# Optimization experiments

Hardware: AMD Instinct MI355X
Metric: run time of the kernel (lower is better)

The kernel has to match this reference:

```python
import jax, jax.numpy as jnp
import numpy as np

N_USER = 100000
N_ITEM = 100000
E = 500000
EMB, HID, OUT = 128, 128, 64


def _mean_agg(msg_src, src, dst, n_dst):
    """Gather per-edge messages from src nodes, segment-mean onto dst nodes."""
    m = msg_src[src]  # [E, d]
    s = jax.ops.segment_sum(m, dst, num_segments=n_dst)
    cnt = jax.ops.segment_sum(jnp.ones((src.shape[0],), m.dtype), dst,
                              num_segments=n_dst)
    # DGL mean reducer yields 0 for nodes with no in-edges
    return jnp.where(cnt[:, None] > 0, s / jnp.maximum(cnt, 1.0)[:, None], 0.0)


def _layer(feat_u, feat_i, W0, b0, Wui, bui, Wiu, biu,
           src_ui, dst_ui, src_iu, dst_iu):
    # shared self-transform (weight0) -> residual h0 on every ntype
    h0_u = feat_u @ W0 + b0
    h0_i = feat_i @ W0 + b0
    # per-etype transform of source features
    wh_u = feat_u @ Wui + bui  # messages along user->item
    wh_i = feat_i @ Wiu + biu  # messages along item->user
    h_i = _mean_agg(wh_u, src_ui, dst_ui, N_ITEM) + h0_i
    h_u = _mean_agg(wh_i, src_iu, dst_iu, N_USER) + h0_u
    return h_u, h_i


def setup_inputs() -> dict:
    key = jax.random.key(0)
    ks = jax.random.split(key, 12)
    sc_e = 1.0 / np.sqrt(EMB)
    sc_h = 1.0 / np.sqrt(HID)
    return {
        "emb_user": jax.random.normal(ks[0], (N_USER, EMB), jnp.float32),
        "emb_item": jax.random.normal(ks[1], (N_ITEM, EMB), jnp.float32),
        "W1_0": jax.random.normal(ks[2], (EMB, HID), jnp.float32) * sc_e,
        "b1_0": jnp.zeros((HID,), jnp.float32),
        "W1_ui": jax.random.normal(ks[3], (EMB, HID), jnp.float32) * sc_e,
        "b1_ui": jnp.zeros((HID,), jnp.float32),
        "W1_iu": jax.random.normal(ks[4], (EMB, HID), jnp.float32) * sc_e,
        "b1_iu": jnp.zeros((HID,), jnp.float32),
        "W2_0": jax.random.normal(ks[5], (HID, OUT), jnp.float32) * sc_h,
        "b2_0": jnp.zeros((OUT,), jnp.float32),
        "W2_ui": jax.random.normal(ks[6], (HID, OUT), jnp.float32) * sc_h,
        "b2_ui": jnp.zeros((OUT,), jnp.float32),
        "W2_iu": jax.random.normal(ks[7], (HID, OUT), jnp.float32) * sc_h,
        "b2_iu": jnp.zeros((OUT,), jnp.float32),
        "src_ui": jax.random.randint(ks[8], (E,), 0, N_USER, jnp.int32),
        "dst_ui": jax.random.randint(ks[9], (E,), 0, N_ITEM, jnp.int32),
        "src_iu": jax.random.randint(ks[10], (E,), 0, N_ITEM, jnp.int32),
        "dst_iu": jax.random.randint(ks[11], (E,), 0, N_USER, jnp.int32),
    }


def reference(emb_user, emb_item,
              W1_0, b1_0, W1_ui, b1_ui, W1_iu, b1_iu,
              W2_0, b2_0, W2_ui, b2_ui, W2_iu, b2_iu,
              src_ui, dst_ui, src_iu, dst_iu):
    h_u, h_i = _layer(emb_user, emb_item, W1_0, b1_0, W1_ui, b1_ui,
                      W1_iu, b1_iu, src_ui, dst_ui, src_iu, dst_iu)
    h_u = jax.nn.leaky_relu(h_u, 0.01)  # torch F.leaky_relu default slope
    h_i = jax.nn.leaky_relu(h_i, 0.01)
    h_u, h_i = _layer(h_u, h_i, W2_0, b2_0, W2_ui, b2_ui,
                      W2_iu, b2_iu, src_ui, dst_ui, src_iu, dst_iu)
    return h_u, h_i
```

## Files before the change

### kernel.cpp

```cpp
#include <hip/hip_runtime.h>

#define N_USER 100000
#define N_ITEM 100000
#define NEDGE  500000
#define DEGCAP 32

typedef __attribute__((ext_vector_type(8))) short short8;
typedef __attribute__((ext_vector_type(4))) float f32x4;

__device__ __forceinline__ unsigned short f2bf(float f) {
  union { float f; unsigned int u; } x{f};
  unsigned int r = x.u + 0x7fffu + ((x.u >> 16) & 1u);
  return (unsigned short)(r >> 16);
}
__device__ __forceinline__ float bf2f(unsigned short u) {
  union { unsigned int u; float f; } x{(unsigned int)u << 16};
  return x.f;
}

__global__ __launch_bounds__(256) void setup_k(
    const int* __restrict__ src_ui, const int* __restrict__ dst_ui,
    int* __restrict__ cur_i, int* __restrict__ csr_ui,
    const int* __restrict__ src_iu, const int* __restrict__ dst_iu,
    int* __restrict__ cur_u, int* __restrict__ csr_iu,
    const float* __restrict__ emb_u, const float* __restrict__ emb_i,
    unsigned short* __restrict__ ebu, unsigned short* __restrict__ ebi,
    const float* __restrict__ W10, const float* __restrict__ W1ui,
    const float* __restrict__ W1iu, const float* __restrict__ W20,
    const float* __restrict__ W2ui, const float* __restrict__ W2iu,
    unsigned short* __restrict__ WT1i, unsigned short* __restrict__ WT1u,
    unsigned short* __restrict__ WT2i, unsigned short* __restrict__ WT2u) {
  int b = blockIdx.x, tid = threadIdx.x;
  if (b < 3908) {
    const int *src, *dst; int *cur, *csr;
    int bb = b;
    if (bb < 1954) { src = src_ui; dst = dst_ui; cur = cur_i; csr = csr_ui; }
    else { bb -= 1954; src = src_iu; dst = dst_iu; cur = cur_u; csr = csr_iu; }
    int e = bb * 256 + tid;
    if (e < NEDGE) {
      int d = dst[e];
      int p = atomicAdd(&cur[d], 1);
      if (p < DEGCAP) csr[d * DEGCAP + p] = src[e];
    }
  } else if (b < 16408) {
    int blk = b - 3908;
    const float* src; unsigned short* dstp;
    if (blk < 6250) { src = emb_u; dstp = ebu; }
    else { blk -= 6250; src = emb_i; dstp = ebi; }
    size_t base = (size_t)blk * 2048 + (size_t)tid * 8;
    float4 x = *(const float4*)(src + base);
    float4 y = *(const float4*)(src + base + 4);
    short8 v{(short)f2bf(x.x), (short)f2bf(x.y), (short)f2bf(x.z), (short)f2bf(x.w),
             (short)f2bf(y.x), (short)f2bf(y.y), (short)f2bf(y.z), (short)f2bf(y.w)};
    *(short8*)(dstp + base) = v;
  } else {
    int t = (b - 16408) * 256 + tid;
    if (t < 32768) {
      int n = t >> 8, k = t & 255;
      float v = (k < 128) ? W10[k * 128 + n] : W1ui[(k - 128) * 128 + n];
      WT1i[t] = f2bf(v);
    } else if (t < 65536) {
      int q = t - 32768; int n = q >> 8, k = q & 255;
      float v = (k < 128) ? W10[k * 128 + n] : W1iu[(k - 128) * 128 + n];
      WT1u[q] = f2bf(v);
    } else if (t < 81920) {
      int q = t - 65536; int n = q >> 8, k = q & 255;
      float v = (k < 128) ? W20[k * 64 + n] : W2ui[(k - 128) * 64 + n];
      WT2i[q] = f2bf(v);
    } else {
      int q = t - 81920; int n = q >> 8, k = q & 255;
      float v = (k < 128) ? W20[k * 64 + n] : W2iu[(k - 128) * 64 + n];
      WT2u[q] = f2bf(v);
    }
  }
}

__global__ __launch_bounds__(256) void agg2_k(
    const unsigned short* __restrict__ featA, const int* __restrict__ curA,
    const int* __restrict__ csrA, unsigned short* __restrict__ outA,
    const unsigned short* __restrict__ featB, const int* __restrict__ curB,
    const int* __restrict__ csrB, unsigned short* __restrict__ outB,
    int nbA) {
  int b = blockIdx.x;
  const unsigned short* feat; const int* cur; const int* csr; unsigned short* out;
  if (b < nbA) { feat = featA; cur = curA; csr = csrA; out = outA; }
  else { b -= nbA; feat = featB; cur = curB; csr = csrB; out = outB; }
  int node = b * 16 + (threadIdx.x >> 4);
  int ln = threadIdx.x & 15;
  int deg = min(cur[node], DEGCAP);
  const int* cp = csr + (size_t)node * DEGCAP;
  float a[8] = {0, 0, 0, 0, 0, 0, 0, 0};
  int j = 0;
  if (j + 4 <= deg) {
    int i0 = cp[0], i1 = cp[1], i2 = cp[2], i3 = cp[3];
    for (;;) {
      bool more = (j + 8 <= deg);
      int n0, n1, n2, n3;
      if (more) { n0 = cp[j + 4]; n1 = cp[j + 5]; n2 = cp[j + 6]; n3 = cp[j + 7]; }
      short8 v0 = *(const short8*)(feat + (size_t)i0 * 128 + ln * 8);
      short8 v1 = *(const short8*)(feat + (size_t)i1 * 128 + ln * 8);
      short8 v2 = *(const short8*)(feat + (size_t)i2 * 128 + ln * 8);
      short8 v3 = *(const short8*)(feat + (size_t)i3 * 128 + ln * 8);
#pragma unroll
      for (int d = 0; d < 8; ++d)
        a[d] += (bf2f((unsigned short)v0[d]) + bf2f((unsigned short)v1[d])) +
                (bf2f((unsigned short)v2[d]) + bf2f((unsigned short)v3[d]));
      j += 4;
      if (!more) break;
      i0 = n0; i1 = n1; i2 = n2; i3 = n3;
    }
  }
  if (j + 2 <= deg) {
    int i0 = cp[j], i1 = cp[j + 1];
    short8 v0 = *(const short8*)(feat + (size_t)i0 * 128 + ln * 8);
    short8 v1 = *(const short8*)(feat + (size_t)i1 * 128 + ln * 8);
#pragma unroll
    for (int d = 0; d < 8; ++d)
      a[d] += bf2f((unsigned short)v0[d]) + bf2f((unsigned short)v1[d]);
    j += 2;
  }
  if (j < deg) {
    short8 v = *(const short8*)(feat + (size_t)cp[j] * 128 + ln * 8);
#pragma unroll
    for (int d = 0; d < 8; ++d) a[d] += bf2f((unsigned short)v[d]);
  }
  float sc = deg ? 1.f / (float)deg : 0.f;
  short8 pk;
#pragma unroll
  for (int d = 0; d < 8; ++d) pk[d] = (short)f2bf(a[d] * sc);
  *(short8*)(out + (size_t)node * 128 + ln * 8) = pk;
}

template <int N, bool LRELU, bool OUTBF16>
__global__ __launch_bounds__(256) void gemm2_k(
    const unsigned short* __restrict__ A1a, const unsigned short* __restrict__ A2a,
    const unsigned short* __restrict__ WTa, const float* __restrict__ b0a,
    const float* __restrict__ bea, const int* __restrict__ cura,
    void* __restrict__ outa,
    const unsigned short* __restrict__ A1b, const unsigned short* __restrict__ A2b,
    const unsigned short* __restrict__ WTb, const float* __restrict__ b0b,
    const float* __restrict__ beb, const int* __restrict__ curb,
    void* __restrict__ outb, int M, int nbA) {
  constexpr int BM = 64;
  constexpr int CPW = N / 4;
  constexpr int NCF = CPW / 16;
  __shared__ short As[BM * 128];
  __shared__ short Ws[N * 128];
  __shared__ float degmask[BM];

  int blk = blockIdx.x;
  const unsigned short* A1; const unsigned short* A2; const unsigned short* WT;
  const float* b0; const float* be; const int* cur; void* outv;
  if (blk < nbA) { A1 = A1a; A2 = A2a; WT = WTa; b0 = b0a; be = bea; cur = cura; outv = outa; }
  else { blk -= nbA; A1 = A1b; A2 = A2b; WT = WTb; b0 = b0b; be = beb; cur = curb; outv = outb; }

  const int tid = threadIdx.x;
  const int lane = tid & 63;
  const int wave = tid >> 6;
  const int row0 = blk * BM;
  const int colbase = wave * CPW;

  if (tid < BM) {
    int r = row0 + tid;
    degmask[tid] = (r < M && cur[r] > 0) ? 1.f : 0.f;
  }

  f32x4 acc[4][NCF] = {};

#pragma unroll
  for (int kh = 0; kh < 2; ++kh) {
    __syncthreads();
    const unsigned short* base = (kh == 0) ? A1 : A2;
#pragma unroll
    for (int it = 0; it < 4; ++it) {
      int chunk = tid + it * 256;
      int row = chunk >> 4, c16 = chunk & 15;
      int gr = row0 + row; if (gr > M - 1) gr = M - 1;
      short8 v = *(const short8*)(base + (size_t)gr * 128 + c16 * 8);
      int byteoff = row * 256 + ((c16 * 16) ^ ((row & 7) << 4));
      *(short8*)((char*)As + byteoff) = v;
    }
#pragma unroll
    for (int it = 0; it < (N * 16) / 256; ++it) {
      int chunk = tid + it * 256;
      int n = chunk >> 4, c16 = chunk & 15;
      short8 v = *(const short8*)(WT + (size_t)n * 256 + kh * 128 + c16 * 8);
      int byteoff = n * 256 + ((c16 * 16) ^ ((n & 7) << 4));
      *(short8*)((char*)Ws + byteoff) = v;
    }
    __syncthreads();

#pragma unroll
    for (int ks = 0; ks < 4; ++ks) {
      short8 af[4];
#pragma unroll
      for (int rf = 0; rf < 4; ++rf) {
        int row = rf * 16 + (lane & 15);
        int c16 = ks * 4 + (lane >> 4);
        int byteoff = row * 256 + ((c16 * 16) ^ ((row & 7) << 4));
        af[rf] = *(const short8*)((const char*)As + byteoff);
      }
      short8 wf[NCF];
#pragma unroll
      for (int cf = 0; cf < NCF; ++cf) {
        int n = colbase + cf * 16 + (lane & 15);
        int c16 = ks * 4 + (lane >> 4);
        int byteoff = n * 256 + ((c16 * 16) ^ ((n & 7) << 4));
        wf[cf] = *(const short8*)((const char*)Ws + byteoff);
      }
#pragma unroll
      for (int rf = 0; rf < 4; ++rf)
#pragma unroll
        for (int cf = 0; cf < NCF; ++cf)
          acc[rf][cf] = __builtin_amdgcn_mfma_f32_16x16x32_bf16(
              af[rf], wf[cf], acc[rf][cf], 0, 0, 0);
    }
  }

#pragma unroll
  for (int cf = 0; cf < NCF; ++cf) {
    int c = colbase + cf * 16 + (lane & 15);
    float bb0 = b0[c], bbe = be[c];
#pragma unroll
    for (int rf = 0; rf < 4; ++rf) {
#pragma unroll
      for (int j = 0; j < 4; ++j) {
        int lr = rf * 16 + (lane >> 4) * 4 + j;
        int r = row0 + lr;
        if (r < M) {
          float v = acc[rf][cf][j] + bb0 + degmask[lr] * bbe;
          if (LRELU) v = (v >= 0.f) ? v : 0.01f * v;
          if (OUTBF16)
            ((unsigned short*)outv)[(size_t)r * N + c] = f2bf(v);
          else
            ((float*)outv)[(size_t)r * N + c] = v;
        }
      }
    }
  }
}

extern "C" void kernel_launch(void* const* d_in, const int* in_sizes, int n_in,
                              void* d_out, int out_size, void* d_ws,
                              size_t ws_size, hipStream_t stream) {
  const float* emb_u = (const float*)d_in[0];
  const float* emb_i = (const float*)d_in[1];
  const float* W1_0  = (const float*)d_in[2];
  const float* b1_0  = (const float*)d_in[3];
  const float* W1_ui = (const float*)d_in[4];
  const float* b1_ui = (const float*)d_in[5];
  const float* W1_iu = (const float*)d_in[6];
  const float* b1_iu = (const float*)d_in[7];
  const float* W2_0  = (const float*)d_in[8];
  const float* b2_0  = (const float*)d_in[9];
  const float* W2_ui = (const float*)d_in[10];
  const float* b2_ui = (const float*)d_in[11];
  const float* W2_iu = (const float*)d_in[12];
  const float* b2_iu = (const float*)d_in[13];
  const int* src_ui = (const int*)d_in[14];
  const int* dst_ui = (const int*)d_in[15];
  const int* src_iu = (const int*)d_in[16];
  const int* dst_iu = (const int*)d_in[17];
  float* out = (float*)d_out;

  char* p = (char*)d_ws;
  unsigned short* WT1i = (unsigned short*)p; p += 65536;
  unsigned short* WT1u = (unsigned short*)p; p += 65536;
  unsigned short* WT2i = (unsigned short*)p; p += 32768;
  unsigned short* WT2u = (unsigned short*)p; p += 32768;
  int* cur_i = (int*)p; p += 400128;
  int* cur_u = (int*)p; p += 400128;
  int* csr_ui = (int*)p; p += (size_t)100032 * DEGCAP * 4;
  int* csr_iu = (int*)p; p += (size_t)100032 * DEGCAP * 4;
  const size_t FB = (size_t)N_USER * 128 * 2;
  unsigned short* ebu  = (unsigned short*)p; p += FB;
  unsigned short* ebi  = (unsigned short*)p; p += FB;
  unsigned short* aggA = (unsigned short*)p; p += FB;
  unsigned short* aggB = (unsigned short*)p; p += FB;
  unsigned short* hu = ebu;
  unsigned short* hi = ebi;

  const int GG = (N_USER + 63) / 64;

  hipMemsetAsync(cur_i, 0, 2 * 400128, stream);
  setup_k<<<16792, 256, 0, stream>>>(src_ui, dst_ui, cur_i, csr_ui,
                                     src_iu, dst_iu, cur_u, csr_iu,
                                     emb_u, emb_i, ebu, ebi,
                                     W1_0, W1_ui, W1_iu, W2_0, W2_ui, W2_iu,
                                     WT1i, WT1u, WT2i, WT2u);

  agg2_k<<<2 * 6250, 256, 0, stream>>>(
      ebu, cur_i, csr_ui, aggA, ebi, cur_u, csr_iu, aggB, 6250);
  gemm2_k<128, true, true><<<2 * GG, 256, 0, stream>>>(
      ebi, aggA, WT1i, b1_0, b1_ui, cur_i, hi,
      ebu, aggB, WT1u, b1_0, b1_iu, cur_u, hu, N_USER, GG);

  agg2_k<<<2 * 6250, 256, 0, stream>>>(
      hu, cur_i, csr_ui, aggA, hi, cur_u, csr_iu, aggB, 6250);
  gemm2_k<64, false, false><<<2 * GG, 256, 0, stream>>>(
      hi, aggA, WT2i, b2_0, b2_ui, cur_i, out + (size_t)N_USER * 64,
      hu, aggB, WT2u, b2_0, b2_iu, cur_u, out, N_USER, GG);
}
```

Before: 253.7 us.

## Move layer-1 self-transform GEMM into setup kernel, interleaved with CSR fill

The layer-1 self term (emb @ W0 + b0) is now computed in the setup kernel, with block indices interleaved across edge-fill, self-GEMM, conversion and weight-transpose roles so the compute-bound GEMM can overlap the atomic-heavy CSR build. The layer-1 GEMM after aggregation then only multiplies the aggregated half (K=128) and adds the precomputed h0, halving its work on the critical path. h0 is staged in the output buffer before that buffer is overwritten by layer 2, and the CSR writes use nontemporal stores. The cost is extra h0 traffic (write plus read back) and a larger, more divergent setup kernel.

```diff
diff --git a/kernel.cpp b/kernel.cpp
--- a/kernel.cpp
+++ b/kernel.cpp
@@ -5,6 +5,12 @@
 #define NEDGE  500000
 #define DEGCAP 32
 
+#define B_FILL 3908
+#define B_GEMM 3126
+#define B_CONV 12500
+#define B_WT   384
+#define B_TOT  (B_FILL + B_GEMM + B_CONV + B_WT)
+
 typedef __attribute__((ext_vector_type(8))) short short8;
 typedef __attribute__((ext_vector_type(4))) float f32x4;
 
@@ -18,7 +24,7 @@
   return x.f;
 }
 
-__global__ __launch_bounds__(256) void setup_k(
+__global__ __launch_bounds__(256, 4) void phase1_k(
     const int* __restrict__ src_ui, const int* __restrict__ dst_ui,
     int* __restrict__ cur_i, int* __restrict__ csr_ui,
     const int* __restrict__ src_iu, const int* __restrict__ dst_iu,
@@ -29,48 +35,121 @@
     const float* __restrict__ W1iu, const float* __restrict__ W20,
     const float* __restrict__ W2ui, const float* __restrict__ W2iu,
     unsigned short* __restrict__ WT1i, unsigned short* __restrict__ WT1u,
-    unsigned short* __restrict__ WT2i, unsigned short* __restrict__ WT2u) {
+    unsigned short* __restrict__ WT2i, unsigned short* __restrict__ WT2u,
+    const float* __restrict__ b10,
+    unsigned short* __restrict__ h0u, unsigned short* __restrict__ h0i) {
+  __shared__ short As[64 * 128];
   int b = blockIdx.x, tid = threadIdx.x;
-  if (b < 3908) {
+  int q = b / 5, m = b % 5;
+
+  if (m == 0 && q < B_FILL) {
     const int *src, *dst; int *cur, *csr;
-    int bb = b;
+    int bb = q;
     if (bb < 1954) { src = src_ui; dst = dst_ui; cur = cur_i; csr = csr_ui; }
     else { bb -= 1954; src = src_iu; dst = dst_iu; cur = cur_u; csr = csr_iu; }
     int e = bb * 256 + tid;
     if (e < NEDGE) {
       int d = dst[e];
       int p = atomicAdd(&cur[d], 1);
-      if (p < DEGCAP) csr[d * DEGCAP + p] = src[e];
-    }
-  } else if (b < 16408) {
-    int blk = b - 3908;
-    const float* src; unsigned short* dstp;
-    if (blk < 6250) { src = emb_u; dstp = ebu; }
-    else { blk -= 6250; src = emb_i; dstp = ebi; }
-    size_t base = (size_t)blk * 2048 + (size_t)tid * 8;
-    float4 x = *(const float4*)(src + base);
-    float4 y = *(const float4*)(src + base + 4);
-    short8 v{(short)f2bf(x.x), (short)f2bf(x.y), (short)f2bf(x.z), (short)f2bf(x.w),
-             (short)f2bf(y.x), (short)f2bf(y.y), (short)f2bf(y.z), (short)f2bf(y.w)};
-    *(short8*)(dstp + base) = v;
+      if (p < DEGCAP) __builtin_nontemporal_store(src[e], &csr[d * DEGCAP + p]);
+    }
+  } else if (m == 1 && q < B_GEMM) {
+    const float* A; unsigned short* h0; int blk;
+    if (q < 1563) { A = emb_i; h0 = h0i; blk = q; }
+    else { A = emb_u; h0 = h0u; blk = q - 1563; }
+    int row0 = blk * 64;
+    int lane = tid & 63, wave = tid >> 6;
+    short8 wf[2][4];
+#pragma unroll
+    for (int cf = 0; cf < 2; ++cf) {
+      int n = wave * 32 + cf * 16 + (lane & 15);
+#pragma unroll
+      for (int ks = 0; ks < 4; ++ks) {
+        int k0 = ks * 32 + (lane >> 4) * 8;
+#pragma unroll
+        for (int j = 0; j < 8; ++j)
+          wf[cf][ks][j] = (short)f2bf(W10[(k0 + j) * 128 + n]);
+      }
+    }
+#pragma unroll
+    for (int it = 0; it < 4; ++it) {
+      int chunk = tid + it * 256;
+      int row = chunk >> 4, c16 = chunk & 15;
+      int gr = row0 + row; if (gr > N_USER - 1) gr = N_USER - 1;
+      const float* s = A + (size_t)gr * 128 + c16 * 8;
+      float4 x = *(const float4*)s;
+      float4 y = *(const float4*)(s + 4);
+      short8 v{(short)f2bf(x.x), (short)f2bf(x.y), (short)f2bf(x.z), (short)f2bf(x.w),
+               (short)f2bf(y.x), (short)f2bf(y.y), (short)f2bf(y.z), (short)f2bf(y.w)};
+      int byteoff = row * 256 + ((c16 * 16) ^ ((row & 7) << 4));
+      *(short8*)((char*)As + byteoff) = v;
+    }
+    __syncthreads();
+    f32x4 acc[4][2] = {};
+#pragma unroll
+    for (int ks = 0; ks < 4; ++ks) {
+      short8 af[4];
+#pragma unroll
+      for (int rf = 0; rf < 4; ++rf) {
+        int row = rf * 16 + (lane & 15);
+        int c16 = ks * 4 + (lane >> 4);
+        int byteoff = row * 256 + ((c16 * 16) ^ ((row & 7) << 4));
+        af[rf] = *(const short8*)((const char*)As + byteoff);
+      }
+#pragma unroll
+      for (int rf = 0; rf < 4; ++rf)
+#pragma unroll
+        for (int cf = 0; cf < 2; ++cf)
+          acc[rf][cf] = __builtin_amdgcn_mfma_f32_16x16x32_bf16(
+              af[rf], wf[cf][ks], acc[rf][cf], 0, 0, 0);
+    }
+#pragma unroll
+    for (int cf = 0; cf < 2; ++cf) {
+      int c = wave * 32 + cf * 16 + (lane & 15);
+      float bb0 = b10[c];
+#pragma unroll
+      for (int rf = 0; rf < 4; ++rf)
+#pragma unroll
+        for (int j = 0; j < 4; ++j) {
+          int r = row0 + rf * 16 + (lane >> 4) * 4 + j;
+          if (r < N_USER)
+            h0[(size_t)r * 128 + c] = f2bf(acc[rf][cf][j] + bb0);
+        }
+    }
   } else {
-    int t = (b - 16408) * 256 + tid;
-    if (t < 32768) {
-      int n = t >> 8, k = t & 255;
-      float v = (k < 128) ? W10[k * 128 + n] : W1ui[(k - 128) * 128 + n];
-      WT1i[t] = f2bf(v);
-    } else if (t < 65536) {
-      int q = t - 32768; int n = q >> 8, k = q & 255;
-      float v = (k < 128) ? W10[k * 128 + n] : W1iu[(k - 128) * 128 + n];
-      WT1u[q] = f2bf(v);
-    } else if (t < 81920) {
-      int q = t - 65536; int n = q >> 8, k = q & 255;
-      float v = (k < 128) ? W20[k * 64 + n] : W2ui[(k - 128) * 64 + n];
-      WT2i[q] = f2bf(v);
+    int fills_before = min((b + 4) / 5, B_FILL);
+    int gems_before  = min((b + 3) / 5, B_GEMM);
+    int sr = b - fills_before - gems_before;
+    if (sr < B_CONV) {
+      int blk = sr;
+      const float* src; unsigned short* dstp;
+      if (blk < 6250) { src = emb_u; dstp = ebu; }
+      else { blk -= 6250; src = emb_i; dstp = ebi; }
+      size_t base = (size_t)blk * 2048 + (size_t)tid * 8;
+      float4 x = *(const float4*)(src + base);
+      float4 y = *(const float4*)(src + base + 4);
+      short8 v{(short)f2bf(x.x), (short)f2bf(x.y), (short)f2bf(x.z), (short)f2bf(x.w),
+               (short)f2bf(y.x), (short)f2bf(y.y), (short)f2bf(y.z), (short)f2bf(y.w)};
+      *(short8*)(dstp + base) = v;
     } else {
-      int q = t - 81920; int n = q >> 8, k = q & 255;
-      float v = (k < 128) ? W20[k * 64 + n] : W2iu[(k - 128) * 64 + n];
-      WT2u[q] = f2bf(v);
+      int t = (sr - B_CONV) * 256 + tid;
+      if (t < 32768) {
+        int n = t >> 8, k = t & 255;
+        float v = (k < 128) ? W10[k * 128 + n] : W1ui[(k - 128) * 128 + n];
+        WT1i[t] = f2bf(v);
+      } else if (t < 65536) {
+        int u = t - 32768; int n = u >> 8, k = u & 255;
+        float v = (k < 128) ? W10[k * 128 + n] : W1iu[(k - 128) * 128 + n];
+        WT1u[u] = f2bf(v);
+      } else if (t < 81920) {
+        int u = t - 65536; int n = u >> 8, k = u & 255;
+        float v = (k < 128) ? W20[k * 64 + n] : W2ui[(k - 128) * 64 + n];
+        WT2i[u] = f2bf(v);
+      } else {
+        int u = t - 81920; int n = u >> 8, k = u & 255;
+        float v = (k < 128) ? W20[k * 64 + n] : W2iu[(k - 128) * 64 + n];
+        WT2u[u] = f2bf(v);
+      }
     }
   }
 }
@@ -131,6 +210,100 @@
   *(short8*)(out + (size_t)node * 128 + ln * 8) = pk;
 }
 
+__global__ __launch_bounds__(256) void egemm_k(
+    const unsigned short* __restrict__ A2a, const unsigned short* __restrict__ h0a,
+    const unsigned short* __restrict__ WTa, const float* __restrict__ bea,
+    const int* __restrict__ cura, unsigned short* __restrict__ outa,
+    const unsigned short* __restrict__ A2b, const unsigned short* __restrict__ h0b,
+    const unsigned short* __restrict__ WTb, const float* __restrict__ beb,
+    const int* __restrict__ curb, unsigned short* __restrict__ outb,
+    int nbA) {
+  __shared__ short As[64 * 128];
+  __shared__ short Ws[128 * 128];
+  __shared__ float degmask[64];
+
+  int blk = blockIdx.x;
+  const unsigned short *A2, *h0, *WT; const float* be; const int* cur;
+  unsigned short* outp;
+  if (blk < nbA) { A2 = A2a; h0 = h0a; WT = WTa; be = bea; cur = cura; outp = outa; }
+  else { blk -= nbA; A2 = A2b; h0 = h0b; WT = WTb; be = beb; cur = curb; outp = outb; }
+
+  const int tid = threadIdx.x;
+  const int lane = tid & 63;
+  const int wave = tid >> 6;
+  const int row0 = blk * 64;
+  const int colbase = wave * 32;
+
+  if (tid < 64) {
+    int r = row0 + tid;
+    degmask[tid] = (r < N_USER && cur[r] > 0) ? 1.f : 0.f;
+  }
+#pragma unroll
+  for (int it = 0; it < 4; ++it) {
+    int chunk = tid + it * 256;
+    int row = chunk >> 4, c16 = chunk & 15;
+    int gr = row0 + row; if (gr > N_USER - 1) gr = N_USER - 1;
+    short8 v = *(const short8*)(A2 + (size_t)gr * 128 + c16 * 8);
+    int byteoff = row * 256 + ((c16 * 16) ^ ((row & 7) << 4));
+    *(short8*)((char*)As + byteoff) = v;
+  }
+#pragma unroll
+  for (int it = 0; it < 8; ++it) {
+    int chunk = tid + it * 256;
+    int n = chunk >> 4, c16 = chunk & 15;
+    short8 v = *(const short8*)(WT + (size_t)n * 256 + 128 + c16 * 8);
+    int byteoff = n * 256 + ((c16 * 16) ^ ((n & 7) << 4));
+    *(short8*)((char*)Ws + byteoff) = v;
+  }
+  __syncthreads();
+
+  f32x4 acc[4][2] = {};
+#pragma unroll
+  for (int ks = 0; ks < 4; ++ks) {
+    short8 af[4];
+#pragma unroll
+    for (int rf = 0; rf < 4; ++rf) {
+      int row = rf * 16 + (lane & 15);
+      int c16 = ks * 4 + (lane >> 4);
+      int byteoff = row * 256 + ((c16 * 16) ^ ((row & 7) << 4));
+      af[rf] = *(const short8*)((const char*)As + byteoff);
+    }
+    short8 wfr[2];
+#pragma unroll
+    for (int cf = 0; cf < 2; ++cf) {
+      int n = colbase + cf * 16 + (lane & 15);
+      int c16 = ks * 4 + (lane >> 4);
+      int byteoff = n * 256 + ((c16 * 16) ^ ((n & 7) << 4));
+      wfr[cf] = *(const short8*)((const char*)Ws + byteoff);
+    }
+#pragma unroll
+    for (int rf = 0; rf < 4; ++rf)
+#pragma unroll
+      for (int cf = 0; cf < 2; ++cf)
+        acc[rf][cf] = __builtin_amdgcn_mfma_f32_16x16x32_bf16(
+            af[rf], wfr[cf], acc[rf][cf], 0, 0, 0);
+  }
+
+#pragma unroll
+  for (int cf = 0; cf < 2; ++cf) {
+    int c = colbase + cf * 16 + (lane & 15);
+    float bbe = be[c];
+#pragma unroll
+    for (int rf = 0; rf < 4; ++rf)
+#pragma unroll
+      for (int j = 0; j < 4; ++j) {
+        int lr = rf * 16 + (lane >> 4) * 4 + j;
+        int r = row0 + lr;
+        if (r < N_USER) {
+          float v = acc[rf][cf][j] + bf2f(h0[(size_t)r * 128 + c]) +
+                    degmask[lr] * bbe;
+          v = (v >= 0.f) ? v : 0.01f * v;
+          outp[(size_t)r * 128 + c] = f2bf(v);
+        }
+      }
+  }
+}
+
 template <int N, bool LRELU, bool OUTBF16>
 __global__ __launch_bounds__(256) void gemm2_k(
     const unsigned short* __restrict__ A1a, const unsigned short* __restrict__ A2a,
@@ -277,27 +450,26 @@
   unsigned short* ebi  = (unsigned short*)p; p += FB;
   unsigned short* aggA = (unsigned short*)p; p += FB;
   unsigned short* aggB = (unsigned short*)p; p += FB;
-  unsigned short* hu = ebu;
-  unsigned short* hi = ebi;
-
-  const int GG = (N_USER + 63) / 64;
+  unsigned short* h0u = (unsigned short*)d_out;
+  unsigned short* h0i = h0u + (size_t)N_USER * 128;
 
   hipMemsetAsync(cur_i, 0, 2 * 400128, stream);
-  setup_k<<<16792, 256, 0, stream>>>(src_ui, dst_ui, cur_i, csr_ui,
-                                     src_iu, dst_iu, cur_u, csr_iu,
-                                     emb_u, emb_i, ebu, ebi,
-                                     W1_0, W1_ui, W1_iu, W2_0, W2_ui, W2_iu,
-                                     WT1i, WT1u, WT2i, WT2u);
+  phase1_k<<<B_TOT, 256, 0, stream>>>(
+      src_ui, dst_ui, cur_i, csr_ui, src_iu, dst_iu, cur_u, csr_iu,
+      emb_u, emb_i, ebu, ebi,
+      W1_0, W1_ui, W1_iu, W2_0, W2_ui, W2_iu,
+      WT1i, WT1u, WT2i, WT2u, b1_0, h0u, h0i);
 
   agg2_k<<<2 * 6250, 256, 0, stream>>>(
       ebu, cur_i, csr_ui, aggA, ebi, cur_u, csr_iu, aggB, 6250);
-  gemm2_k<128, true, true><<<2 * GG, 256, 0, stream>>>(
-      ebi, aggA, WT1i, b1_0, b1_ui, cur_i, hi,
-      ebu, aggB, WT1u, b1_0, b1_iu, cur_u, hu, N_USER, GG);
+  egemm_k<<<2 * 1563, 256, 0, stream>>>(
+      aggA, h0i, WT1i, b1_ui, cur_i, ebi,
+      aggB, h0u, WT1u, b1_iu, cur_u, ebu,
+      1563);
 
   agg2_k<<<2 * 6250, 256, 0, stream>>>(
-      hu, cur_i, csr_ui, aggA, hi, cur_u, csr_iu, aggB, 6250);
-  gemm2_k<64, false, false><<<2 * GG, 256, 0, stream>>>(
-      hi, aggA, WT2i, b2_0, b2_ui, cur_i, out + (size_t)N_USER * 64,
-      hu, aggB, WT2u, b2_0, b2_iu, cur_u, out, N_USER, GG);
-}
+      ebu, cur_i, csr_ui, aggA, ebi, cur_u, csr_iu, aggB, 6250);
+  gemm2_k<64, false, false><<<2 * 1563, 256, 0, stream>>>(
+      ebi, aggA, WT2i, b2_0, b2_ui, cur_i, out + (size_t)N_USER * 64,
+      ebu, aggB, WT2u, b2_0, b2_iu, cur_u, out, N_USER, 1563);
+}
```

Result: slower. 279.8 us (+10.3%).

## Shard CSR build counters into four replicas and compact neighbor lists in LDS

Applied to the files above, without the earlier changes.

The CSR build now spreads each destination's atomic counter across four replicas, each with its own 16-slot bucket. Each thread handles four edges and writes neighbors with nontemporal stores, and setup blocks are scrambled so fill, convert and weight-transpose work interleave. The aggregation kernel loads the 64-slot row, prefix-scans the replica counts within each 16-lane group, and compacts the indices into LDS before gathering. The aggregation scratch buffers now alias the output buffer, which cuts workspace traffic but depends on each GEMM block reading its aggregated rows before overwriting the same bytes.

```diff
diff --git a/kernel.cpp b/kernel.cpp
--- a/kernel.cpp
+++ b/kernel.cpp
@@ -3,7 +3,13 @@
 #define N_USER 100000
 #define N_ITEM 100000
 #define NEDGE  500000
-#define DEGCAP 32
+#define CURS   100032
+#define RCAP   16
+
+#define B_FILL 978
+#define B_CONV 12500
+#define B_WT   384
+#define B_TOT  (B_FILL + B_CONV + B_WT)
 
 typedef __attribute__((ext_vector_type(8))) short short8;
 typedef __attribute__((ext_vector_type(4))) float f32x4;
@@ -30,31 +36,48 @@
     const float* __restrict__ W2ui, const float* __restrict__ W2iu,
     unsigned short* __restrict__ WT1i, unsigned short* __restrict__ WT1u,
     unsigned short* __restrict__ WT2i, unsigned short* __restrict__ WT2u) {
-  int b = blockIdx.x, tid = threadIdx.x;
-  if (b < 3908) {
+  int b = (int)(((unsigned long long)blockIdx.x * 7919ull) % (unsigned long long)B_TOT);
+  int tid = threadIdx.x;
+  if (b < B_FILL) {
     const int *src, *dst; int *cur, *csr;
     int bb = b;
-    if (bb < 1954) { src = src_ui; dst = dst_ui; cur = cur_i; csr = csr_ui; }
-    else { bb -= 1954; src = src_iu; dst = dst_iu; cur = cur_u; csr = csr_iu; }
-    int e = bb * 256 + tid;
-    if (e < NEDGE) {
-      int d = dst[e];
-      int p = atomicAdd(&cur[d], 1);
-      if (p < DEGCAP) csr[d * DEGCAP + p] = src[e];
-    }
-  } else if (b < 16408) {
-    int blk = b - 3908;
+    if (bb < 489) { src = src_ui; dst = dst_ui; cur = cur_i; csr = csr_ui; }
+    else { bb -= 489; src = src_iu; dst = dst_iu; cur = cur_u; csr = csr_iu; }
+    int e0 = bb * 1024 + tid;
+    int d[4], s[4];
+    bool ok[4];
+#pragma unroll
+    for (int k = 0; k < 4; ++k) {
+      int e = e0 + k * 256;
+      ok[k] = (e < NEDGE);
+      d[k] = ok[k] ? dst[e] : 0;
+      s[k] = ok[k] ? src[e] : 0;
+    }
+    int p[4];
+#pragma unroll
+    for (int k = 0; k < 4; ++k) {
+      int rk = (tid + k) & 3;
+      p[k] = ok[k] ? atomicAdd(&cur[rk * CURS + d[k]], 1) : RCAP;
+    }
+#pragma unroll
+    for (int k = 0; k < 4; ++k) {
+      int rk = (tid + k) & 3;
+      if (ok[k] && p[k] < RCAP)
+        __builtin_nontemporal_store(s[k], &csr[d[k] * 64 + rk * RCAP + p[k]]);
+    }
+  } else if (b < B_FILL + B_CONV) {
+    int blk = b - B_FILL;
     const float* src; unsigned short* dstp;
     if (blk < 6250) { src = emb_u; dstp = ebu; }
     else { blk -= 6250; src = emb_i; dstp = ebi; }
-    size_t base = (size_t)blk * 2048 + (size_t)tid * 8;
-    float4 x = *(const float4*)(src + base);
-    float4 y = *(const float4*)(src + base + 4);
+    size_t g = (size_t)blk * 2048 + (size_t)tid * 8;
+    float4 x = *(const float4*)(src + g);
+    float4 y = *(const float4*)(src + g + 4);
     short8 v{(short)f2bf(x.x), (short)f2bf(x.y), (short)f2bf(x.z), (short)f2bf(x.w),
              (short)f2bf(y.x), (short)f2bf(y.y), (short)f2bf(y.z), (short)f2bf(y.w)};
-    *(short8*)(dstp + base) = v;
+    *(short8*)(dstp + g) = v;
   } else {
-    int t = (b - 16408) * 256 + tid;
+    int t = (b - B_FILL - B_CONV) * 256 + tid;
     if (t < 32768) {
       int n = t >> 8, k = t & 255;
       float v = (k < 128) ? W10[k * 128 + n] : W1ui[(k - 128) * 128 + n];
@@ -75,28 +98,49 @@
   }
 }
 
-__global__ __launch_bounds__(256) void agg2_k(
+__global__ __launch_bounds__(256) void aggc_k(
     const unsigned short* __restrict__ featA, const int* __restrict__ curA,
     const int* __restrict__ csrA, unsigned short* __restrict__ outA,
     const unsigned short* __restrict__ featB, const int* __restrict__ curB,
     const int* __restrict__ csrB, unsigned short* __restrict__ outB,
     int nbA) {
+  __shared__ int sidx[16][64];
   int b = blockIdx.x;
   const unsigned short* feat; const int* cur; const int* csr; unsigned short* out;
   if (b < nbA) { feat = featA; cur = curA; csr = csrA; out = outA; }
   else { b -= nbA; feat = featB; cur = curB; csr = csrB; out = outB; }
-  int node = b * 16 + (threadIdx.x >> 4);
-  int ln = threadIdx.x & 15;
-  int deg = min(cur[node], DEGCAP);
-  const int* cp = csr + (size_t)node * DEGCAP;
+  int grp = threadIdx.x >> 4;
+  int ln  = threadIdx.x & 15;
+  int node = b * 16 + grp;
+
+  int4 sl = *(const int4*)(csr + (size_t)node * 64 + ln * 4);
+  int cr = cur[(size_t)(ln >> 2) * CURS + node];
+  cr = min(cr, RCAP);
+  int m = cr - (ln & 3) * 4;
+  m = m < 0 ? 0 : (m > 4 ? 4 : m);
+  int pre = m;
+#pragma unroll
+  for (int d = 1; d < 16; d <<= 1) {
+    int t = __shfl_up(pre, d, 16);
+    if (ln >= d) pre += t;
+  }
+  int start = pre - m;
+  int deg = __shfl(pre, 15, 16);
+  if (m > 0) sidx[grp][start] = sl.x;
+  if (m > 1) sidx[grp][start + 1] = sl.y;
+  if (m > 2) sidx[grp][start + 2] = sl.z;
+  if (m > 3) sidx[grp][start + 3] = sl.w;
+  __syncthreads();
+
+  const int* lidx = sidx[grp];
   float a[8] = {0, 0, 0, 0, 0, 0, 0, 0};
   int j = 0;
   if (j + 4 <= deg) {
-    int i0 = cp[0], i1 = cp[1], i2 = cp[2], i3 = cp[3];
+    int i0 = lidx[0], i1 = lidx[1], i2 = lidx[2], i3 = lidx[3];
     for (;;) {
       bool more = (j + 8 <= deg);
       int n0, n1, n2, n3;
-      if (more) { n0 = cp[j + 4]; n1 = cp[j + 5]; n2 = cp[j + 6]; n3 = cp[j + 7]; }
+      if (more) { n0 = lidx[j + 4]; n1 = lidx[j + 5]; n2 = lidx[j + 6]; n3 = lidx[j + 7]; }
       short8 v0 = *(const short8*)(feat + (size_t)i0 * 128 + ln * 8);
       short8 v1 = *(const short8*)(feat + (size_t)i1 * 128 + ln * 8);
       short8 v2 = *(const short8*)(feat + (size_t)i2 * 128 + ln * 8);
@@ -111,7 +155,7 @@
     }
   }
   if (j + 2 <= deg) {
-    int i0 = cp[j], i1 = cp[j + 1];
+    int i0 = lidx[j], i1 = lidx[j + 1];
     short8 v0 = *(const short8*)(feat + (size_t)i0 * 128 + ln * 8);
     short8 v1 = *(const short8*)(feat + (size_t)i1 * 128 + ln * 8);
 #pragma unroll
@@ -120,7 +164,7 @@
     j += 2;
   }
   if (j < deg) {
-    short8 v = *(const short8*)(feat + (size_t)cp[j] * 128 + ln * 8);
+    short8 v = *(const short8*)(feat + (size_t)lidx[j] * 128 + ln * 8);
 #pragma unroll
     for (int d = 0; d < 8; ++d) a[d] += bf2f((unsigned short)v[d]);
   }
@@ -162,7 +206,10 @@
 
   if (tid < BM) {
     int r = row0 + tid;
-    degmask[tid] = (r < M && cur[r] > 0) ? 1.f : 0.f;
+    int ds = 0;
+    if (r < M)
+      ds = cur[r] + cur[CURS + r] + cur[2 * CURS + r] + cur[3 * CURS + r];
+    degmask[tid] = (ds > 0) ? 1.f : 0.f;
   }
 
   f32x4 acc[4][NCF] = {};
@@ -268,34 +315,34 @@
   unsigned short* WT1u = (unsigned short*)p; p += 65536;
   unsigned short* WT2i = (unsigned short*)p; p += 32768;
   unsigned short* WT2u = (unsigned short*)p; p += 32768;
-  int* cur_i = (int*)p; p += 400128;
-  int* cur_u = (int*)p; p += 400128;
-  int* csr_ui = (int*)p; p += (size_t)100032 * DEGCAP * 4;
-  int* csr_iu = (int*)p; p += (size_t)100032 * DEGCAP * 4;
+  int* cur_i = (int*)p; p += 4 * CURS * 4;
+  int* cur_u = (int*)p; p += 4 * CURS * 4;
+  int* csr_ui = (int*)p; p += (size_t)CURS * 64 * 4;
+  int* csr_iu = (int*)p; p += (size_t)CURS * 64 * 4;
   const size_t FB = (size_t)N_USER * 128 * 2;
   unsigned short* ebu  = (unsigned short*)p; p += FB;
   unsigned short* ebi  = (unsigned short*)p; p += FB;
-  unsigned short* aggA = (unsigned short*)p; p += FB;
-  unsigned short* aggB = (unsigned short*)p; p += FB;
   unsigned short* hu = ebu;
   unsigned short* hi = ebi;
+  unsigned short* aggB = (unsigned short*)out;
+  unsigned short* aggA = (unsigned short*)(out + (size_t)N_USER * 64);
 
   const int GG = (N_USER + 63) / 64;
 
-  hipMemsetAsync(cur_i, 0, 2 * 400128, stream);
-  setup_k<<<16792, 256, 0, stream>>>(src_ui, dst_ui, cur_i, csr_ui,
+  hipMemsetAsync(cur_i, 0, 2 * 4 * CURS * 4, stream);
+  setup_k<<<B_TOT, 256, 0, stream>>>(src_ui, dst_ui, cur_i, csr_ui,
                                      src_iu, dst_iu, cur_u, csr_iu,
                                      emb_u, emb_i, ebu, ebi,
                                      W1_0, W1_ui, W1_iu, W2_0, W2_ui, W2_iu,
                                      WT1i, WT1u, WT2i, WT2u);
 
-  agg2_k<<<2 * 6250, 256, 0, stream>>>(
+  aggc_k<<<2 * 6250, 256, 0, stream>>>(
       ebu, cur_i, csr_ui, aggA, ebi, cur_u, csr_iu, aggB, 6250);
   gemm2_k<128, true, true><<<2 * GG, 256, 0, stream>>>(
       ebi, aggA, WT1i, b1_0, b1_ui, cur_i, hi,
       ebu, aggB, WT1u, b1_0, b1_iu, cur_u, hu, N_USER, GG);
 
-  agg2_k<<<2 * 6250, 256, 0, stream>>>(
+  aggc_k<<<2 * 6250, 256, 0, stream>>>(
       hu, cur_i, csr_ui, aggA, hi, cur_u, csr_iu, aggB, 6250);
   gemm2_k<64, false, false><<<2 * GG, 256, 0, stream>>>(
       hi, aggA, WT2i, b2_0, b2_ui, cur_i, out + (size_t)N_USER * 64,
```

Result: faster. 240.3 us (-5.3%).
